# Kernel tuning notes

Hardware: AMD Instinct MI355X
Metric: run time of the kernel (lower is better)

Reference implementation:

```python
import jax, jax.numpy as jnp
import numpy as np

N, E, B, D, OUT = 15000, 60000, 512, 64, 12
NI, EI, EH = 15, 5, 128
STEPS = 6  # both num_step_message_passing and num_step_set2set


def setup_inputs():
    key = jax.random.key(0)
    ks = jax.random.split(key, 30)
    r = lambda k, s, sc=0.05: jax.random.normal(k, s, jnp.float32) * sc
    return {
        "x": r(ks[0], (N, NI), 1.0),
        "edge_attr": r(ks[1], (E, EI), 1.0),
        "edge_index": jax.random.randint(ks[2], (2, E), 0, N),
        "batch": jnp.sort(jax.random.randint(ks[3], (N,), 0, B)),
        "lin0_w": r(ks[4], (D, NI)), "lin0_b": r(ks[5], (D,)),
        "en_w1": r(ks[6], (EH, EI)), "en_b1": r(ks[7], (EH,)),
        "en_w2": r(ks[8], (D * D, EH)), "en_b2": r(ks[9], (D * D,)),
        "conv_b": r(ks[10], (D,)),
        "gru_w_ih": r(ks[11], (3 * D, D)), "gru_w_hh": r(ks[12], (3 * D, D)),
        "gru_b_ih": r(ks[13], (3 * D,)), "gru_b_hh": r(ks[14], (3 * D,)),
        "lstm_w_ih": r(ks[15], (4 * D, 2 * D)), "lstm_w_hh": r(ks[16], (4 * D, D)),
        "lstm_b_ih": r(ks[17], (4 * D,)), "lstm_b_hh": r(ks[18], (4 * D,)),
        "lin1_w": r(ks[19], (D, 2 * D)), "lin1_b": r(ks[20], (D,)),
        "lin2_w": r(ks[21], (OUT, D)), "lin2_b": r(ks[22], (OUT,)),
    }


def _forward(x, edge_attr, lin0_w, lin0_b, en_w1, en_b1, en_w2, en_b2, conv_b,
             gru_w_ih, gru_w_hh, gru_b_ih, gru_b_hh,
             lstm_w_ih, lstm_w_hh, lstm_b_ih, lstm_b_hh,
             lin1_w, lin1_b, lin2_w, lin2_b, edge_index, batch):
    src, tgt = edge_index[0], edge_index[1]
    deg = jnp.maximum(jax.ops.segment_sum(jnp.ones((E,), x.dtype), tgt, num_segments=N), 1.0)
    # NNConv edge network (edge_attr is constant across MP steps -> hoist; same math)
    ew = jax.nn.relu(edge_attr @ en_w1.T + en_b1) @ en_w2.T + en_b2
    ew = ew.reshape(E, D, D)  # [E, in, out] per-edge weight matrices

    out = jax.nn.relu(x @ lin0_w.T + lin0_b)  # lin0
    h = out  # GRU hidden state (num_layers=1, seq_len=1)
    for _ in range(STEPS):
        # gather -> per-edge matvec -> scatter-mean (NNConv, aggr='mean', root_weight=False)
        msg = jnp.einsum('ei,eio->eo', out[src], ew)
        agg = jax.ops.segment_sum(msg, tgt, num_segments=N) / deg[:, None]
        m = jax.nn.relu(agg + conv_b)
        # single GRU step (PyTorch gate layout: r, z, n)
        gi = m @ gru_w_ih.T + gru_b_ih
        gh = h @ gru_w_hh.T + gru_b_hh
        ir, iz, inn = jnp.split(gi, 3, axis=-1)
        hr, hz, hn = jnp.split(gh, 3, axis=-1)
        rg = jax.nn.sigmoid(ir + hr)
        zg = jax.nn.sigmoid(iz + hz)
        ng = jnp.tanh(inn + rg * hn)
        h = (1.0 - zg) * ng + zg * h
        out = h

    # Set2Set pooling (LSTM gate layout: i, f, g, o)
    q_star = jnp.zeros((B, 2 * D), x.dtype)
    hl = jnp.zeros((B, D), x.dtype)
    cl = jnp.zeros((B, D), x.dtype)
    for _ in range(STEPS):
        g = q_star @ lstm_w_ih.T + lstm_b_ih + hl @ lstm_w_hh.T + lstm_b_hh
        ig, fg, gg, og = jnp.split(g, 4, axis=-1)
        cl = jax.nn.sigmoid(fg) * cl + jax.nn.sigmoid(ig) * jnp.tanh(gg)
        hl = jax.nn.sigmoid(og) * jnp.tanh(cl)
        e = jnp.sum(out * hl[batch], axis=-1)  # [N] attention logits
        emax = jax.ops.segment_max(e, batch, num_segments=B)
        ex = jnp.exp(e - emax[batch])
        denom = jax.ops.segment_sum(ex, batch, num_segments=B)
        a = ex / (denom[batch] + 1e-16)  # batch-segmented softmax
        rvec = jax.ops.segment_sum(a[:, None] * out, batch, num_segments=B)
        q_star = jnp.concatenate([hl, rvec], axis=-1)

    y = jax.nn.relu(q_star @ lin1_w.T + lin1_b) @ lin2_w.T + lin2_b
    return y  # [B, OUT]


def reference(x, edge_attr, edge_index, batch, lin0_w, lin0_b, en_w1, en_b1, en_w2, en_b2,
              conv_b, gru_w_ih, gru_w_hh, gru_b_ih, gru_b_hh,
              lstm_w_ih, lstm_w_hh, lstm_b_ih, lstm_b_hh, lin1_w, lin1_b, lin2_w, lin2_b):
    return _forward(x, edge_attr, lin0_w, lin0_b, en_w1, en_b1, en_w2, en_b2, conv_b,
                    gru_w_ih, gru_w_hh, gru_b_ih, gru_b_hh,
                    lstm_w_ih, lstm_w_hh, lstm_b_ih, lstm_b_hh,
                    lin1_w, lin1_b, lin2_w, lin2_b, edge_index, batch)
```

## Files before the change

kernel.cpp:

```cpp
#include <hip/hip_runtime.h>
#include <hip/hip_bf16.h>
#include <math.h>

#define NN 15000
#define NE 60000
#define NB 512
#define NIF 15
#define EIF 5
#define EHID 128
#define NSTEP 6
#define EPB 128

typedef _Float16 half8 __attribute__((ext_vector_type(8)));
typedef float floatx4 __attribute__((ext_vector_type(4)));

typedef __attribute__((address_space(3))) _Float16 lds_f16;
typedef __attribute__((address_space(1))) const _Float16 glb_f16;

__device__ __forceinline__ void gload_lds16(const _Float16* g, _Float16* l) {
  __builtin_amdgcn_global_load_lds((glb_f16*)g, (lds_f16*)l, 16, 0, 0);
}

__device__ __forceinline__ float sigmoidf_(float x) { return 1.f / (1.f + expf(-x)); }

__global__ void k_sentinel(float* out) { out[0] = 1000.0f; }

__global__ void k_init(const float* __restrict__ x, const float* __restrict__ l0w,
                       const float* __restrict__ l0b, const int* __restrict__ tgt,
                       const int* __restrict__ batch, float* __restrict__ outv,
                       float* __restrict__ deg, int* __restrict__ gstart,
                       int* __restrict__ gend,
                       const float* __restrict__ ea, const float* __restrict__ w1,
                       const float* __restrict__ b1,
                       const float* __restrict__ w2, const float* __restrict__ b2,
                       const float* __restrict__ gwih, const float* __restrict__ gwhh,
                       const float* __restrict__ lwih, const float* __restrict__ lwhh,
                       _Float16* __restrict__ w2pp, _Float16* __restrict__ hidp,
                       _Float16* __restrict__ wgpk,
                       float* __restrict__ wTih, float* __restrict__ wThh) {
  int idx = blockIdx.x * 256 + threadIdx.x;
  if (idx < NN * 64) {
    int n = idx >> 6, d = idx & 63;
    float s = l0b[d];
#pragma unroll
    for (int i = 0; i < NIF; ++i) s += x[n * NIF + i] * l0w[d * NIF + i];
    outv[idx] = fmaxf(s, 0.f);
  }
  if (idx < NE) atomicAdd(&deg[tgt[idx]], 1.0f);
  if (idx < NN) {
    int bb = batch[idx];
    atomicMin(&gstart[bb], idx);
    atomicMax(&gend[bb], idx + 1);
  }
  {
    int ih = idx - NN * 64;
    if (ih >= 0 && ih < NE * 16) {
      int e = ih >> 4, part = ih & 15;
      float eav[EIF];
#pragma unroll
      for (int i = 0; i < EIF; ++i) eav[i] = ea[e * EIF + i];
      half8 hv;
#pragma unroll
      for (int j = 0; j < 8; ++j) {
        int h = part * 8 + j;
        float s = b1[h];
#pragma unroll
        for (int i = 0; i < EIF; ++i) s += eav[i] * w1[h * EIF + i];
        hv[j] = (_Float16)fmaxf(s, 0.f);
      }
      *(half8*)&hidp[(size_t)e * 128 + part * 8] = hv;
    }
  }
  if (idx < 528384) {
    int g = idx >> 9;
    int r = idx & 511;
    int o = r >> 3, j = r & 7;
    float v;
    if (g < 1024) {
      int i = g >> 4;
      int h = ((g & 15) << 3) + j;
      v = w2[(size_t)(i * 64 + o) * 128 + h];
    } else {
      int i = ((g - 1024) << 3) + j;
      v = b2[i * 64 + o];
    }
    w2pp[idx] = (_Float16)v;
  } else if (idx < 528384 + 24576) {
    int i2 = idx - 528384;
    int kc = i2 / 6144;
    int rem = i2 % 6144;
    int o = rem >> 5, r = rem & 31;
    int kind = kc >> 1, cc = kc & 1;
    float v = kind ? gwhh[o * 64 + cc * 32 + r] : gwih[o * 64 + cc * 32 + r];
    wgpk[i2] = (_Float16)v;
  } else if (idx < 528384 + 24576 + 32768) {
    int i3 = idx - (528384 + 24576);
    int k = i3 >> 8, g = i3 & 255;
    wTih[i3] = lwih[g * 128 + k];
  } else if (idx < 528384 + 24576 + 32768 + 16384) {
    int i4 = idx - (528384 + 24576 + 32768);
    int k = i4 >> 8, g = i4 & 255;
    wThh[i4] = lwhh[g * 64 + k];
  }
}

__global__ __launch_bounds__(256, 5) void k_msg(
    const float* __restrict__ outv, const _Float16* __restrict__ hidp,
    const _Float16* __restrict__ w2pp, const int* __restrict__ src,
    const int* __restrict__ tgt, float* __restrict__ agg) {
  __shared__ __align__(16) _Float16 osL[EPB][40];
  __shared__ __align__(16) _Float16 bS[2][4096];
  int tid = threadIdx.x;
  int e0 = blockIdx.x * EPB;
  int ib = blockIdx.y >> 1, hb = blockIdx.y & 1;
  const int cbase = ib * 128 + hb * 2;

  int el = tid >> 1, hf = tid & 1;
  int e = e0 + el;
  bool valid = e < NE;
  int s = valid ? src[e] : 0;
  const float4* op = (const float4*)(outv + (size_t)s * 64 + ib * 32);
  {
    float4 v0 = op[hf * 4 + 0];
    float4 v1 = op[hf * 4 + 1];
    float4 v2 = op[hf * 4 + 2];
    float4 v3 = op[hf * 4 + 3];
    if (!valid) {
      v0 = v1 = v2 = v3 = make_float4(0.f, 0.f, 0.f, 0.f);
    }
    half8 p0, p1;
    p0[0] = (_Float16)v0.x; p0[1] = (_Float16)v0.y;
    p0[2] = (_Float16)v0.z; p0[3] = (_Float16)v0.w;
    p0[4] = (_Float16)v1.x; p0[5] = (_Float16)v1.y;
    p0[6] = (_Float16)v1.z; p0[7] = (_Float16)v1.w;
    p1[0] = (_Float16)v2.x; p1[1] = (_Float16)v2.y;
    p1[2] = (_Float16)v2.z; p1[3] = (_Float16)v2.w;
    p1[4] = (_Float16)v3.x; p1[5] = (_Float16)v3.y;
    p1[6] = (_Float16)v3.z; p1[7] = (_Float16)v3.w;
    *(half8*)&osL[el][hf * 16 + 0] = p0;
    *(half8*)&osL[el][hf * 16 + 8] = p1;
  }

  int wv = tid >> 6, lane = tid & 63;
  int l15 = lane & 15, q = lane >> 4;
  int rbase = wv * 32 + l15;

  half8 hidf[2][2];
#pragma unroll
  for (int m = 0; m < 2; ++m) {
    int ef = e0 + rbase + m * 16;
    if (ef > NE - 1) ef = NE - 1;
    const _Float16* hp = hidp + (size_t)ef * 128 + hb * 64 + q * 8;
    hidf[m][0] = *(const half8*)hp;
    hidf[m][1] = *(const half8*)(hp + 32);
  }

  __syncthreads();

  {
    const _Float16* g0 = w2pp + (size_t)cbase * 2048 + tid * 8;
    gload_lds16(g0, &bS[0][0] + tid * 8);
    gload_lds16(g0 + 2048, &bS[0][0] + tid * 8 + 2048);
    const _Float16* g1 = w2pp + (size_t)(cbase + 4) * 2048 + tid * 8;
    gload_lds16(g1, &bS[1][0] + tid * 8);
    gload_lds16(g1 + 2048, &bS[1][0] + tid * 8 + 2048);
  }

  floatx4 acc[2][4];
#pragma unroll
  for (int m = 0; m < 2; ++m)
#pragma unroll
    for (int og = 0; og < 4; ++og) acc[m][og] = (floatx4){0.f, 0.f, 0.f, 0.f};

  const int fbase = q * 512 + l15 * 8;

  for (int il = 0; il < 32; ++il) {
    int p = il & 1;
    _Float16 osv0 = osL[rbase][il];
    _Float16 osv1 = osL[rbase + 16][il];
    if (il < 31) {
      asm volatile("s_waitcnt vmcnt(2)" ::: "memory");
    } else {
      asm volatile("s_waitcnt vmcnt(0)" ::: "memory");
    }
    __builtin_amdgcn_s_barrier();
    half8 fr[2][4];
    const _Float16* bb = &bS[p][0];
#pragma unroll
    for (int hc = 0; hc < 2; ++hc)
#pragma unroll
      for (int og = 0; og < 4; ++og)
        fr[hc][og] = *(const half8*)&bb[hc * 2048 + fbase + og * 128];
    asm volatile("s_waitcnt lgkmcnt(0)" ::: "memory");
    __builtin_amdgcn_sched_barrier(0);
    __builtin_amdgcn_s_barrier();
    if (il < 30) {
      const _Float16* gsrc = w2pp + (size_t)(cbase + (il + 2) * 4) * 2048 + tid * 8;
      _Float16* ldst = &bS[p][0] + tid * 8;
      gload_lds16(gsrc, ldst);
      gload_lds16(gsrc + 2048, ldst + 2048);
    }
    half8 os0 = {osv0, osv0, osv0, osv0, osv0, osv0, osv0, osv0};
    half8 os1 = {osv1, osv1, osv1, osv1, osv1, osv1, osv1, osv1};
#pragma unroll
    for (int hc = 0; hc < 2; ++hc) {
      half8 af0 = hidf[0][hc] * os0;
      half8 af1 = hidf[1][hc] * os1;
#pragma unroll
      for (int og = 0; og < 4; ++og) {
        acc[0][og] = __builtin_amdgcn_mfma_f32_16x16x32_f16(af0, fr[hc][og], acc[0][og], 0, 0, 0);
        acc[1][og] = __builtin_amdgcn_mfma_f32_16x16x32_f16(af1, fr[hc][og], acc[1][og], 0, 0, 0);
      }
    }
  }

  if (hb == 0) {
    int cb = 256 + ib;
    const _Float16* bp = w2pp + ((size_t)(cb * 4 + q) * 64 + l15) * 8;
    half8 af[2];
#pragma unroll
    for (int m = 0; m < 2; ++m)
      af[m] = *(const half8*)&osL[rbase + m * 16][q * 8];
#pragma unroll
    for (int og = 0; og < 4; ++og) {
      half8 bf = *(const half8*)(bp + og * 128);
#pragma unroll
      for (int m = 0; m < 2; ++m)
        acc[m][og] = __builtin_amdgcn_mfma_f32_16x16x32_f16(af[m], bf, acc[m][og], 0, 0, 0);
    }
  }

#pragma unroll
  for (int m = 0; m < 2; ++m) {
    int erow = e0 + wv * 32 + m * 16 + q * 4;
#pragma unroll
    for (int j = 0; j < 4; ++j) {
      int ee = erow + j;
      if (ee < NE) {
        int t = tgt[ee];
        float* ap = agg + (size_t)t * 64 + l15;
#pragma unroll
        for (int og = 0; og < 4; ++og) atomicAdd(ap + og * 16, acc[m][og][j]);
      }
    }
  }
}

__global__ __launch_bounds__(128, 2) void k_gru(
    float* __restrict__ agg, const float* __restrict__ deg,
    const float* __restrict__ convb, const _Float16* __restrict__ wgpk,
    const float* __restrict__ bih, const float* __restrict__ bhh,
    float* __restrict__ outv) {
  __shared__ __align__(16) _Float16 aL[32][136];
  __shared__ float hF[32][68];
  __shared__ float cbL[64];
  int tid = threadIdx.x;
  int n0 = blockIdx.x * 32;
  if (tid < 64) cbL[tid] = convb[tid];
  __syncthreads();

  int nl = tid >> 2, dq = (tid & 3) * 16;
  int n = n0 + nl;
  if (n < NN) {
    float dg = fmaxf(deg[n], 1.f);
    const float4* ap = (const float4*)(agg + (size_t)n * 64 + dq);
    const float4* hp = (const float4*)(outv + (size_t)n * 64 + dq);
    float4* az = (float4*)(agg + (size_t)n * 64 + dq);
#pragma unroll
    for (int t = 0; t < 4; ++t) {
      float4 a = ap[t];
      float4 h = hp[t];
      int d = dq + t * 4;
      aL[nl][d + 0] = (_Float16)fmaxf(a.x / dg + cbL[d + 0], 0.f);
      aL[nl][d + 1] = (_Float16)fmaxf(a.y / dg + cbL[d + 1], 0.f);
      aL[nl][d + 2] = (_Float16)fmaxf(a.z / dg + cbL[d + 2], 0.f);
      aL[nl][d + 3] = (_Float16)fmaxf(a.w / dg + cbL[d + 3], 0.f);
      aL[nl][64 + d + 0] = (_Float16)h.x;
      aL[nl][64 + d + 1] = (_Float16)h.y;
      aL[nl][64 + d + 2] = (_Float16)h.z;
      aL[nl][64 + d + 3] = (_Float16)h.w;
      hF[nl][d + 0] = h.x; hF[nl][d + 1] = h.y;
      hF[nl][d + 2] = h.z; hF[nl][d + 3] = h.w;
      az[t] = make_float4(0.f, 0.f, 0.f, 0.f);
    }
  } else {
#pragma unroll
    for (int t = 0; t < 4; ++t) {
      int d = dq + t * 4;
#pragma unroll
      for (int u = 0; u < 4; ++u) {
        aL[nl][d + u] = (_Float16)0.f;
        aL[nl][64 + d + u] = (_Float16)0.f;
        hF[nl][d + u] = 0.f;
      }
    }
  }
  __syncthreads();

  int wv = tid >> 6, lane = tid & 63, l15 = lane & 15, qd = lane >> 4;
  floatx4 acc[2][6][2];
#pragma unroll
  for (int mt = 0; mt < 2; ++mt)
#pragma unroll
    for (int t6 = 0; t6 < 6; ++t6)
#pragma unroll
      for (int kind = 0; kind < 2; ++kind) acc[mt][t6][kind] = (floatx4){0.f, 0.f, 0.f, 0.f};

#pragma unroll
  for (int kind = 0; kind < 2; ++kind) {
#pragma unroll
    for (int cc = 0; cc < 2; ++cc) {
      half8 af[2];
#pragma unroll
      for (int mt = 0; mt < 2; ++mt)
        af[mt] = *(const half8*)&aL[mt * 16 + l15][kind * 64 + cc * 32 + qd * 8];
#pragma unroll
      for (int t6 = 0; t6 < 6; ++t6) {
        int gb = (t6 * 2 + wv) * 16;
        half8 bf = *(const half8*)&wgpk[((size_t)(kind * 2 + cc) * 192 + gb + l15) * 32 + qd * 8];
#pragma unroll
        for (int mt = 0; mt < 2; ++mt)
          acc[mt][t6][kind] = __builtin_amdgcn_mfma_f32_16x16x32_f16(af[mt], bf, acc[mt][t6][kind], 0, 0, 0);
      }
    }
  }

#pragma unroll
  for (int dd = 0; dd < 2; ++dd) {
    int d = (dd * 2 + wv) * 16 + l15;
    float bir = bih[d], bhr = bhh[d];
    float biz = bih[64 + d], bhz = bhh[64 + d];
    float bin = bih[128 + d], bhn = bhh[128 + d];
#pragma unroll
    for (int mt = 0; mt < 2; ++mt) {
#pragma unroll
      for (int j = 0; j < 4; ++j) {
        int nloc = mt * 16 + qd * 4 + j;
        int nn = n0 + nloc;
        if (nn < NN) {
          float ir = acc[mt][dd][0][j] + bir, hr = acc[mt][dd][1][j] + bhr;
          float iz = acc[mt][2 + dd][0][j] + biz, hz = acc[mt][2 + dd][1][j] + bhz;
          float in_ = acc[mt][4 + dd][0][j] + bin, hn = acc[mt][4 + dd][1][j] + bhn;
          float r = sigmoidf_(ir + hr);
          float z = sigmoidf_(iz + hz);
          float ng = tanhf(in_ + r * hn);
          float h = hF[nloc][d];
          outv[(size_t)nn * 64 + d] = (1.f - z) * ng + z * h;
        }
      }
    }
  }
}

__global__ __launch_bounds__(256) void k_s2s(
    const float* __restrict__ outv, const int* __restrict__ gstart,
    const int* __restrict__ gend, const float* __restrict__ wTih,
    const float* __restrict__ wThh, const float* __restrict__ bih,
    const float* __restrict__ bhh, const float* __restrict__ l1w,
    const float* __restrict__ l1b, const float* __restrict__ l2w,
    const float* __restrict__ l2b, float* __restrict__ y) {
  __shared__ float qL[128], hlL[64], clL[64], gL[256];
  __shared__ float mxA[4], smA[4], accA[4][64], hidL[64];
  int b = blockIdx.x, tid = threadIdx.x, wv = tid >> 6, lane = tid & 63;
  int s0 = gstart[b], e0 = gend[b];
  if (s0 > e0) { s0 = 0; e0 = 0; }
  if (tid < 128) qL[tid] = 0.f;
  if (tid < 64) { hlL[tid] = 0.f; clL[tid] = 0.f; }
  __syncthreads();

  for (int step = 0; step < NSTEP; ++step) {
    {
      int g = tid;
      float s = bih[g] + bhh[g];
      for (int k = 0; k < 128; ++k) s += qL[k] * wTih[k * 256 + g];
      for (int k = 0; k < 64; ++k) s += hlL[k] * wThh[k * 256 + g];
      gL[g] = s;
    }
    __syncthreads();
    if (tid < 64) {
      float ig = gL[tid], fg = gL[64 + tid], gg = gL[128 + tid], og = gL[192 + tid];
      float c = sigmoidf_(fg) * clL[tid] + sigmoidf_(ig) * tanhf(gg);
      clL[tid] = c;
      hlL[tid] = sigmoidf_(og) * tanhf(c);
    }
    __syncthreads();
    float hd = hlL[lane];
    float mxw = -1e30f;
    for (int nn = s0 + wv; nn < e0; nn += 4) {
      float v = outv[(size_t)nn * 64 + lane] * hd;
#pragma unroll
      for (int off = 32; off > 0; off >>= 1) v += __shfl_xor(v, off);
      mxw = fmaxf(mxw, v);
    }
    if (lane == 0) mxA[wv] = mxw;
    __syncthreads();
    float mx = fmaxf(fmaxf(mxA[0], mxA[1]), fmaxf(mxA[2], mxA[3]));
    float sm = 0.f, ac = 0.f;
    for (int nn = s0 + wv; nn < e0; nn += 4) {
      float o_nd = outv[(size_t)nn * 64 + lane];
      float v = o_nd * hd;
#pragma unroll
      for (int off = 32; off > 0; off >>= 1) v += __shfl_xor(v, off);
      float ex = expf(v - mx);
      sm += ex;
      ac += ex * o_nd;
    }
    if (lane == 0) smA[wv] = sm;
    accA[wv][lane] = ac;
    __syncthreads();
    if (tid < 64) {
      float den = smA[0] + smA[1] + smA[2] + smA[3] + 1e-16f;
      float rv = (accA[0][tid] + accA[1][tid] + accA[2][tid] + accA[3][tid]) / den;
      qL[tid] = hlL[tid];
      qL[64 + tid] = rv;
    }
    __syncthreads();
  }
  if (tid < 64) {
    float s = l1b[tid];
    for (int k = 0; k < 128; ++k) s += qL[k] * l1w[tid * 128 + k];
    hidL[tid] = fmaxf(s, 0.f);
  }
  __syncthreads();
  if (tid < 12) {
    float s = l2b[tid];
    for (int k = 0; k < 64; ++k) s += hidL[k] * l2w[tid * 64 + k];
    y[b * 12 + tid] = s;
  }
}

extern "C" void kernel_launch(void* const* d_in, const int* in_sizes, int n_in,
                              void* d_out, int out_size, void* d_ws, size_t ws_size,
                              hipStream_t stream) {
  const float* x = (const float*)d_in[0];
  const float* ea = (const float*)d_in[1];
  const int* eidx = (const int*)d_in[2];
  const int* batch = (const int*)d_in[3];
  const float* lin0_w = (const float*)d_in[4];
  const float* lin0_b = (const float*)d_in[5];
  const float* en_w1 = (const float*)d_in[6];
  const float* en_b1 = (const float*)d_in[7];
  const float* en_w2 = (const float*)d_in[8];
  const float* en_b2 = (const float*)d_in[9];
  const float* conv_b = (const float*)d_in[10];
  const float* gru_wih = (const float*)d_in[11];
  const float* gru_whh = (const float*)d_in[12];
  const float* gru_bih = (const float*)d_in[13];
  const float* gru_bhh = (const float*)d_in[14];
  const float* lstm_wih = (const float*)d_in[15];
  const float* lstm_whh = (const float*)d_in[16];
  const float* lstm_bih = (const float*)d_in[17];
  const float* lstm_bhh = (const float*)d_in[18];
  const float* lin1_w = (const float*)d_in[19];
  const float* lin1_b = (const float*)d_in[20];
  const float* lin2_w = (const float*)d_in[21];
  const float* lin2_b = (const float*)d_in[22];
  const int* srcp = eidx;
  const int* tgtp = eidx + NE;

  char* ws = (char*)d_ws;
  size_t off = 0;
  auto alloc = [&](size_t bytes) {
    char* p = ws + off;
    off += (bytes + 255) & ~(size_t)255;
    return p;
  };
  _Float16* w2pp = (_Float16*)alloc((size_t)1032 * 512 * 2);
  _Float16* hidp = (_Float16*)alloc((size_t)NE * 128 * 2);
  _Float16* wgpk = (_Float16*)alloc((size_t)24576 * 2);
  float* wTih = (float*)alloc((size_t)32768 * 4);
  float* wThh = (float*)alloc((size_t)16384 * 4);
  float* out = (float*)alloc((size_t)NN * 64 * 4);
  float* agg = (float*)alloc((size_t)NN * 64 * 4);
  float* deg = (float*)alloc((size_t)NN * 4);
  int* gstart = (int*)alloc((size_t)NB * 4);
  int* gend = (int*)alloc((size_t)NB * 4);
  if (off > ws_size) {
    k_sentinel<<<1, 1, 0, stream>>>((float*)d_out);
    return;
  }

  hipMemsetAsync(deg, 0, (size_t)NN * 4, stream);
  hipMemsetAsync(gstart, 0x7f, (size_t)NB * 4, stream);
  hipMemsetAsync(gend, 0, (size_t)NB * 4, stream);
  hipMemsetAsync(agg, 0, (size_t)NN * 64 * 4, stream);

  k_init<<<(NN * 64 + NE * 16 + 255) / 256, 256, 0, stream>>>(
      x, lin0_w, lin0_b, tgtp, batch, out, deg, gstart, gend,
      ea, en_w1, en_b1, en_w2, en_b2, gru_wih, gru_whh, lstm_wih, lstm_whh,
      w2pp, hidp, wgpk, wTih, wThh);

  for (int step = 0; step < NSTEP; ++step) {
    k_msg<<<dim3((NE + EPB - 1) / EPB, 4), 256, 0, stream>>>(out, hidp, w2pp,
                                                             srcp, tgtp, agg);
    k_gru<<<(NN + 31) / 32, 128, 0, stream>>>(agg, deg, conv_b, wgpk, gru_bih,
                                              gru_bhh, out);
  }

  k_s2s<<<NB, 256, 0, stream>>>(out, gstart, gend, wTih, wThh, lstm_bih, lstm_bhh,
                                lin1_w, lin1_b, lin2_w, lin2_b, (float*)d_out);
}
```

Baseline: 753.0 us.

## Merge input-dimension split in k_msg so each block covers all 64 inputs

Removes the split of the 64-wide input dimension across blocks in the message kernel. Each block now loops over all 64 input channels, with the grid y-dimension cut from 4 to 2. This halves the atomicAdd scatter traffic into agg and the redundant per-edge hidden-feature loads, at the cost of half as many blocks, longer serial loops, a larger LDS tile, and a lower occupancy hint.

```diff
diff --git a/kernel.cpp b/kernel.cpp
--- a/kernel.cpp
+++ b/kernel.cpp
@@ -104,41 +104,33 @@
   }
 }
 
-__global__ __launch_bounds__(256, 5) void k_msg(
+__global__ __launch_bounds__(256, 4) void k_msg(
     const float* __restrict__ outv, const _Float16* __restrict__ hidp,
     const _Float16* __restrict__ w2pp, const int* __restrict__ src,
     const int* __restrict__ tgt, float* __restrict__ agg) {
-  __shared__ __align__(16) _Float16 osL[EPB][40];
+  __shared__ __align__(16) _Float16 osL[EPB][72];
   __shared__ __align__(16) _Float16 bS[2][4096];
   int tid = threadIdx.x;
   int e0 = blockIdx.x * EPB;
-  int ib = blockIdx.y >> 1, hb = blockIdx.y & 1;
-  const int cbase = ib * 128 + hb * 2;
+  int hb = blockIdx.y;
+  const int cbase = hb * 2;
 
   int el = tid >> 1, hf = tid & 1;
   int e = e0 + el;
   bool valid = e < NE;
   int s = valid ? src[e] : 0;
-  const float4* op = (const float4*)(outv + (size_t)s * 64 + ib * 32);
-  {
-    float4 v0 = op[hf * 4 + 0];
-    float4 v1 = op[hf * 4 + 1];
-    float4 v2 = op[hf * 4 + 2];
-    float4 v3 = op[hf * 4 + 3];
-    if (!valid) {
-      v0 = v1 = v2 = v3 = make_float4(0.f, 0.f, 0.f, 0.f);
-    }
-    half8 p0, p1;
-    p0[0] = (_Float16)v0.x; p0[1] = (_Float16)v0.y;
-    p0[2] = (_Float16)v0.z; p0[3] = (_Float16)v0.w;
-    p0[4] = (_Float16)v1.x; p0[5] = (_Float16)v1.y;
-    p0[6] = (_Float16)v1.z; p0[7] = (_Float16)v1.w;
-    p1[0] = (_Float16)v2.x; p1[1] = (_Float16)v2.y;
-    p1[2] = (_Float16)v2.z; p1[3] = (_Float16)v2.w;
-    p1[4] = (_Float16)v3.x; p1[5] = (_Float16)v3.y;
-    p1[6] = (_Float16)v3.z; p1[7] = (_Float16)v3.w;
-    *(half8*)&osL[el][hf * 16 + 0] = p0;
-    *(half8*)&osL[el][hf * 16 + 8] = p1;
+  const float4* op = (const float4*)(outv + (size_t)s * 64 + hf * 32);
+#pragma unroll
+  for (int pr = 0; pr < 4; ++pr) {
+    float4 va = op[pr * 2 + 0];
+    float4 vb = op[pr * 2 + 1];
+    if (!valid) { va = vb = make_float4(0.f, 0.f, 0.f, 0.f); }
+    half8 pk;
+    pk[0] = (_Float16)va.x; pk[1] = (_Float16)va.y;
+    pk[2] = (_Float16)va.z; pk[3] = (_Float16)va.w;
+    pk[4] = (_Float16)vb.x; pk[5] = (_Float16)vb.y;
+    pk[6] = (_Float16)vb.z; pk[7] = (_Float16)vb.w;
+    *(half8*)&osL[el][hf * 32 + pr * 8] = pk;
   }
 
   int wv = tid >> 6, lane = tid & 63;
@@ -174,11 +166,11 @@
 
   const int fbase = q * 512 + l15 * 8;
 
-  for (int il = 0; il < 32; ++il) {
+  for (int il = 0; il < 64; ++il) {
     int p = il & 1;
     _Float16 osv0 = osL[rbase][il];
     _Float16 osv1 = osL[rbase + 16][il];
-    if (il < 31) {
+    if (il < 63) {
       asm volatile("s_waitcnt vmcnt(2)" ::: "memory");
     } else {
       asm volatile("s_waitcnt vmcnt(0)" ::: "memory");
@@ -194,7 +186,7 @@
     asm volatile("s_waitcnt lgkmcnt(0)" ::: "memory");
     __builtin_amdgcn_sched_barrier(0);
     __builtin_amdgcn_s_barrier();
-    if (il < 30) {
+    if (il < 62) {
       const _Float16* gsrc = w2pp + (size_t)(cbase + (il + 2) * 4) * 2048 + tid * 8;
       _Float16* ldst = &bS[p][0] + tid * 8;
       gload_lds16(gsrc, ldst);
@@ -215,18 +207,21 @@
   }
 
   if (hb == 0) {
-    int cb = 256 + ib;
-    const _Float16* bp = w2pp + ((size_t)(cb * 4 + q) * 64 + l15) * 8;
-    half8 af[2];
-#pragma unroll
-    for (int m = 0; m < 2; ++m)
-      af[m] = *(const half8*)&osL[rbase + m * 16][q * 8];
-#pragma unroll
-    for (int og = 0; og < 4; ++og) {
-      half8 bf = *(const half8*)(bp + og * 128);
+#pragma unroll
+    for (int ibb = 0; ibb < 2; ++ibb) {
+      int cb = 256 + ibb;
+      const _Float16* bp = w2pp + ((size_t)(cb * 4 + q) * 64 + l15) * 8;
+      half8 af[2];
 #pragma unroll
       for (int m = 0; m < 2; ++m)
-        acc[m][og] = __builtin_amdgcn_mfma_f32_16x16x32_f16(af[m], bf, acc[m][og], 0, 0, 0);
+        af[m] = *(const half8*)&osL[rbase + m * 16][ibb * 32 + q * 8];
+#pragma unroll
+      for (int og = 0; og < 4; ++og) {
+        half8 bf = *(const half8*)(bp + og * 128);
+#pragma unroll
+        for (int m = 0; m < 2; ++m)
+          acc[m][og] = __builtin_amdgcn_mfma_f32_16x16x32_f16(af[m], bf, acc[m][og], 0, 0, 0);
+      }
     }
   }
 
@@ -491,7 +486,7 @@
       w2pp, hidp, wgpk, wTih, wThh);
 
   for (int step = 0; step < NSTEP; ++step) {
-    k_msg<<<dim3((NE + EPB - 1) / EPB, 4), 256, 0, stream>>>(out, hidp, w2pp,
+    k_msg<<<dim3((NE + EPB - 1) / EPB, 2), 256, 0, stream>>>(out, hidp, w2pp,
                                                              srcp, tgtp, agg);
     k_gru<<<(NN + 31) / 32, 128, 0, stream>>>(agg, deg, conv_b, wgpk, gru_bih,
                                               gru_bhh, out);
```

After: 692.8 us. -8.0%, faster.
